# Kernel optimization log

Measured on AMD Instinct MI355X. Metric: run time of the kernel, lower is better.

## Reference

```python
import jax, jax.numpy as jnp
import numpy as np

N = 100_000      # target ('paper') nodes
E_RAND = 500_000 # random metapath edges (self-loops added on top)
C = 256          # channels
H = 8            # heads
D = C // H       # proj_dim = 32
SEM = 128        # semantic attention hidden
NEG_SLOPE = 0.2


def _edges(k):
    e = jax.random.randint(k, (2, E_RAND), 0, N, dtype=jnp.int32)
    loops = jnp.broadcast_to(jnp.arange(N, dtype=jnp.int32), (2, N))
    return jnp.concatenate([e, loops], axis=1)  # [2, E_RAND + N]


def setup_inputs() -> dict:
    key = jax.random.key(0)
    ks = jax.random.split(key, 9)
    return {
        "x": jax.random.normal(ks[0], (N, C), dtype=jnp.float32),
        "W": jax.random.normal(ks[1], (D, C), dtype=jnp.float32) * (1.0 / np.sqrt(C)),
        "att1": jax.random.normal(ks[2], (H, 2 * D), dtype=jnp.float32) * (1.0 / np.sqrt(2 * D)),
        "att2": jax.random.normal(ks[3], (H, 2 * D), dtype=jnp.float32) * (1.0 / np.sqrt(2 * D)),
        "fc_w": jax.random.normal(ks[4], (SEM, C), dtype=jnp.float32) * (1.0 / np.sqrt(C)),
        "fc_b": jnp.zeros((SEM,), dtype=jnp.float32),
        "q": jax.random.normal(ks[5], (SEM,), dtype=jnp.float32) * (1.0 / np.sqrt(SEM)),
        "ei1": _edges(ks[6]),
        "ei2": _edges(ks[7]),
    }


def _segment_softmax(e, dst, num_nodes):
    # numerically stable softmax over edges grouped by destination node
    m = jax.ops.segment_max(e, dst, num_segments=num_nodes)      # [N, H]
    ex = jnp.exp(e - m[dst])                                     # [E, H]
    s = jax.ops.segment_sum(ex, dst, num_segments=num_nodes)     # [N, H]
    return ex / s[dst]


def _gat_layer(h, ei, att):
    # h: [N, d] projected target features; ei: [2, E]; att: [H, 2d]
    src, dst = ei[0], ei[1]
    n, d = h.shape
    a_dst, a_src = att[:, :d], att[:, d:]   # cat order in torch: [h_i(dst), h_j(src)]
    # per-edge attention logits [E, H] without materializing [E, H, 2d]
    e = jax.nn.leaky_relu(h[dst] @ a_dst.T + h[src] @ a_src.T, NEG_SLOPE)
    alpha = _segment_softmax(e, dst, n)                          # [E, H]
    m = h[src][:, None, :] * alpha[:, :, None]                   # [E, H, d]
    out = jax.ops.segment_sum(m, dst, num_segments=n)            # [N, H, d]
    return jax.nn.elu(out).reshape(n, H * d)                     # [N, H*d]


def reference(x, W, att1, att2, fc_w, fc_b, q, ei1, ei2):
    # type-specific projection (bias-free Linear): [N, C] -> [N, d]
    h = x @ W.T
    Z1 = _gat_layer(h, ei1, att1)
    Z2 = _gat_layer(h, ei2, att2)
    # semantic attention across meta-paths
    def score(Z):
        return (jnp.tanh(Z @ fc_w.T + fc_b) @ q).mean()
    V = jax.nn.softmax(jnp.stack([score(Z1), score(Z2)]))        # [2]
    return V[0] * Z1 + V[1] * Z2                                 # [N, C]
```

## Files before the change

### kernel.cpp

```cpp
#include <hip/hip_runtime.h>
#include <math.h>

#define Nn 100000
#define Cc 256
#define Dd 32
#define Hh 8
#define SEMk 128
#define PAD 32
#define NEG 0.2f
#define NB1 25000
#define NTASK 12500

#if __has_builtin(__builtin_amdgcn_exp2f)
#define EXP2(x) __builtin_amdgcn_exp2f(x)
#else
#define EXP2(x) exp2f(x)
#endif
#define LOG2E 1.44269504088896f

typedef __attribute__((ext_vector_type(8))) short bf16x8;
typedef __attribute__((ext_vector_type(4))) short s16x4;
typedef __attribute__((ext_vector_type(4))) float f32x4;

__device__ __forceinline__ short f2bf(float f) {
    unsigned u = __float_as_uint(f);
    u = (u + 0x7FFF + ((u >> 16) & 1)) >> 16;
    return (short)u;
}

__global__ __launch_bounds__(256) void k_prep(const float* __restrict__ W,
                                              float* __restrict__ Wt,
                                              const float* __restrict__ fcw,
                                              short* __restrict__ fcwb) {
    int i = blockIdx.x * 256 + threadIdx.x;
    if (i < Dd * Cc) {
        int j = i >> 5, k = i & 31;
        Wt[i] = W[k * Cc + j];
    }
    if (i < SEMk * Cc) fcwb[i] = f2bf(fcw[i]);
}

__global__ __launch_bounds__(256) void k_hproj(const float* __restrict__ x,
                                               const float* __restrict__ Wt,
                                               const float* __restrict__ att1,
                                               const float* __restrict__ att2,
                                               float* __restrict__ h,
                                               float* __restrict__ sd1, float* __restrict__ ss1,
                                               float* __restrict__ sd2, float* __restrict__ ss2) {
    __shared__ float4 xs[32 * 65];
    __shared__ float  wt[256 * 36];
    __shared__ float4 hs[32 * 9];
    __shared__ float  a1[8 * 68];
    __shared__ float  a2[8 * 68];

    int t = threadIdx.x;
    int nb = blockIdx.x * 32;

    const float4* xg = (const float4*)x + (size_t)nb * 64;
#pragma unroll
    for (int it = 0; it < 8; ++it) {
        int i = t + it * 256;
        xs[(i >> 6) * 65 + (i & 63)] = xg[i];
    }
    const float4* wg = (const float4*)Wt;
#pragma unroll
    for (int it = 0; it < 8; ++it) {
        int i = t + it * 256;
        *(float4*)&wt[(i >> 3) * 36 + (i & 7) * 4] = wg[i];
    }
#pragma unroll
    for (int it = 0; it < 2; ++it) {
        int i = t + it * 256;
        a1[(i >> 6) * 68 + (i & 63)] = att1[i];
        a2[(i >> 6) * 68 + (i & 63)] = att2[i];
    }
    __syncthreads();

    int nl = t >> 3;
    int dq = t & 7;
    float4 acc = make_float4(0.f, 0.f, 0.f, 0.f);
    const float4* xr = &xs[nl * 65];
#pragma unroll 4
    for (int j4 = 0; j4 < 64; ++j4) {
        float4 xv = xr[j4];
        float4 w0 = *(const float4*)&wt[(j4 * 4 + 0) * 36 + dq * 4];
        float4 w1 = *(const float4*)&wt[(j4 * 4 + 1) * 36 + dq * 4];
        float4 w2 = *(const float4*)&wt[(j4 * 4 + 2) * 36 + dq * 4];
        float4 w3 = *(const float4*)&wt[(j4 * 4 + 3) * 36 + dq * 4];
        acc.x += xv.x * w0.x + xv.y * w1.x + xv.z * w2.x + xv.w * w3.x;
        acc.y += xv.x * w0.y + xv.y * w1.y + xv.z * w2.y + xv.w * w3.y;
        acc.z += xv.x * w0.z + xv.y * w1.z + xv.z * w2.z + xv.w * w3.z;
        acc.w += xv.x * w0.w + xv.y * w1.w + xv.z * w2.w + xv.w * w3.w;
    }
    ((float4*)h)[(size_t)(nb + nl) * 8 + dq] = acc;
    hs[nl * 9 + dq] = acc;
    __syncthreads();

    int nl2 = t >> 3;
    int hh = t & 7;
    float d1 = 0.f, s1 = 0.f, d2 = 0.f, s2 = 0.f;
#pragma unroll
    for (int d4 = 0; d4 < 8; ++d4) {
        float4 hv = hs[nl2 * 9 + d4];
        float4 ad1 = *(const float4*)&a1[hh * 68 + d4 * 4];
        float4 as1 = *(const float4*)&a1[hh * 68 + 32 + d4 * 4];
        float4 ad2 = *(const float4*)&a2[hh * 68 + d4 * 4];
        float4 as2 = *(const float4*)&a2[hh * 68 + 32 + d4 * 4];
        d1 += hv.x * ad1.x + hv.y * ad1.y + hv.z * ad1.z + hv.w * ad1.w;
        s1 += hv.x * as1.x + hv.y * as1.y + hv.z * as1.z + hv.w * as1.w;
        d2 += hv.x * ad2.x + hv.y * ad2.y + hv.z * ad2.z + hv.w * ad2.w;
        s2 += hv.x * as2.x + hv.y * as2.y + hv.z * as2.z + hv.w * as2.w;
    }
    int n = nb + nl2;
    sd1[n * 8 + hh] = d1 * LOG2E; ss1[n * 8 + hh] = s1 * LOG2E;
    sd2[n * 8 + hh] = d2 * LOG2E; ss2[n * 8 + hh] = s2 * LOG2E;
}

__global__ __launch_bounds__(256) void k_scatter(const int* __restrict__ ei1, int E1,
                                                 const int* __restrict__ ei2, int E2,
                                                 int* __restrict__ cnt,
                                                 int* __restrict__ slt1,
                                                 int* __restrict__ slt2) {
    int id = blockIdx.x * 256 + threadIdx.x;
    const int* ei; int e, EE; int* c; int* sl;
    if (id < E1) { ei = ei1; e = id; EE = E1; c = cnt; sl = slt1; }
    else {
        e = id - E1;
        if (e >= E2) return;
        ei = ei2; EE = E2; c = cnt + Nn; sl = slt2;
    }
    int s = ei[e];
    int d = ei[EE + e];
    int pos = atomicAdd(&c[d], 1);
    if (pos < PAD) sl[d * PAD + pos] = s;
}

#define LOADC(S0,S1,S2,S3,A0,A1,A2,A3,V0,V1,V2,V3,BB) do {                         \
    S0 = __shfl(sval, (BB) + 0); S1 = __shfl(sval, (BB) + 1);                      \
    S2 = __shfl(sval, (BB) + 2); S3 = __shfl(sval, (BB) + 3);                      \
    S1 = ((BB) + 1 < deg) ? S1 : n;                                                \
    S2 = ((BB) + 2 < deg) ? S2 : n;                                                \
    S3 = ((BB) + 3 < deg) ? S3 : n;                                                \
    A0 = ssrc[(unsigned)S0 * 8u + hh]; A1 = ssrc[(unsigned)S1 * 8u + hh];          \
    A2 = ssrc[(unsigned)S2 * 8u + hh]; A3 = ssrc[(unsigned)S3 * 8u + hh];          \
    V0 = h4[(unsigned)S0 * 8u + sub];  V1 = h4[(unsigned)S1 * 8u + sub];           \
    V2 = h4[(unsigned)S2 * 8u + sub];  V3 = h4[(unsigned)S3 * 8u + sub];           \
} while (0)

#define CONS(A0,A1,A2,A3,V0,V1,V2,V3,BB) do {                                      \
    float ev_, w_;                                                                 \
    ev_ = sd + A0; ev_ = ev_ > 0.f ? ev_ : NEG * ev_; w_ = EXP2(ev_);              \
    acc.x += w_ * V0.x; acc.y += w_ * V0.y; acc.z += w_ * V0.z; acc.w += w_ * V0.w; ssum += w_; \
    ev_ = sd + A1; ev_ = ev_ > 0.f ? ev_ : NEG * ev_; w_ = EXP2(ev_);              \
    w_ = ((BB) + 1 < deg) ? w_ : 0.f;                                              \
    acc.x += w_ * V1.x; acc.y += w_ * V1.y; acc.z += w_ * V1.z; acc.w += w_ * V1.w; ssum += w_; \
    ev_ = sd + A2; ev_ = ev_ > 0.f ? ev_ : NEG * ev_; w_ = EXP2(ev_);              \
    w_ = ((BB) + 2 < deg) ? w_ : 0.f;                                              \
    acc.x += w_ * V2.x; acc.y += w_ * V2.y; acc.z += w_ * V2.z; acc.w += w_ * V2.w; ssum += w_; \
    ev_ = sd + A3; ev_ = ev_ > 0.f ? ev_ : NEG * ev_; w_ = EXP2(ev_);              \
    w_ = ((BB) + 3 < deg) ? w_ : 0.f;                                              \
    acc.x += w_ * V3.x; acc.y += w_ * V3.y; acc.z += w_ * V3.z; acc.w += w_ * V3.w; ssum += w_; \
} while (0)

__global__ __launch_bounds__(256, 4) void k_gat(const float* __restrict__ h,
                                                const float* __restrict__ sd1, const float* __restrict__ ss1,
                                                const float* __restrict__ sd2, const float* __restrict__ ss2,
                                                const int* __restrict__ cnt,
                                                const int* __restrict__ slt1, const int* __restrict__ slt2,
                                                float* __restrict__ Z1, float* __restrict__ Z2) {
    int blk = blockIdx.x;
    const float* sdst = sd1; const float* ssrc = ss1;
    const int* cc = cnt; const int* sl = slt1; float* Z = Z1;
    if (blk >= NB1) { blk -= NB1; sdst = sd2; ssrc = ss2; cc = cnt + Nn; sl = slt2; Z = Z2; }
    int t = threadIdx.x;
    int lane = t & 63;
    int n = blk * 4 + (t >> 6);
    int deg = cc[n]; if (deg > PAD) deg = PAD;
    int hh = lane >> 3;
    int sub = lane & 7;
    float sd = sdst[n * 8 + hh];
    int sval = sl[n * PAD + (lane & 31)];
    const float4* h4 = (const float4*)h;

    float ssum = 0.f;
    float4 acc = make_float4(0.f, 0.f, 0.f, 0.f);

    int as0, as1, as2, as3;  float aa0, aa1, aa2, aa3;  float4 av0, av1, av2, av3;
    int bs0, bs1, bs2, bs3;  float ba0, ba1, ba2, ba3;  float4 bv0, bv1, bv2, bv3;

    LOADC(as0, as1, as2, as3, aa0, aa1, aa2, aa3, av0, av1, av2, av3, 0);
    int base = 0;
    for (;;) {
        int nxt = base + 4;
        bool more = nxt < deg;
        if (more) LOADC(bs0, bs1, bs2, bs3, ba0, ba1, ba2, ba3, bv0, bv1, bv2, bv3, nxt);
        CONS(aa0, aa1, aa2, aa3, av0, av1, av2, av3, base);
        if (!more) break;
        base = nxt;
        nxt = base + 4;
        more = nxt < deg;
        if (more) LOADC(as0, as1, as2, as3, aa0, aa1, aa2, aa3, av0, av1, av2, av3, nxt);
        CONS(ba0, ba1, ba2, ba3, bv0, bv1, bv2, bv3, base);
        if (!more) break;
        base = nxt;
    }

    float inv = 1.f / ssum;
    float4 o;
    o.x = acc.x * inv; o.y = acc.y * inv; o.z = acc.z * inv; o.w = acc.w * inv;
    o.x = o.x > 0.f ? o.x : __expf(o.x) - 1.f;
    o.y = o.y > 0.f ? o.y : __expf(o.y) - 1.f;
    o.z = o.z > 0.f ? o.z : __expf(o.z) - 1.f;
    o.w = o.w > 0.f ? o.w : __expf(o.w) - 1.f;
    ((float4*)Z)[(size_t)n * 64 + lane] = o;
}

__device__ __forceinline__ float fast_tanh(float x) {
    return 1.f - 2.f / (1.f + __expf(2.f * x));
}

#define SWZ(off, r) ((off) ^ (((r) & 7) << 4))

__global__ __launch_bounds__(256) void k_score(const float* __restrict__ Z1,
                        const float* __restrict__ Z2,
                        const short* __restrict__ fcwb,
                        const float* __restrict__ fcb,
                        const float* __restrict__ q,
                        float* __restrict__ Sacc) {
    __shared__ float zst[4 * 4096];
    int t = threadIdx.x;
    int lane = t & 63;
    int wid = t >> 6;
    int task = blockIdx.x * 4 + wid;
    const float* Z = Z1; float* bins = Sacc;
    int tile = task;
    if (task >= NTASK / 2) { Z = Z2; bins = Sacc + 256; tile = task - NTASK / 2; }
    int nodebase = tile * 16;
    float* myst = &zst[wid * 4096];

    const char* zb = (const char*)(Z + (size_t)nodebase * Cc);
#pragma unroll
    for (int r = 0; r < 16; ++r) {
        const char* src = zb + r * 1024 + SWZ(lane * 16, r);
        __builtin_amdgcn_global_load_lds(
            (const __attribute__((address_space(1))) void*)src,
            (__attribute__((address_space(3))) void*)(myst + r * 256),
            16, 0, 0);
    }
    asm volatile("s_waitcnt vmcnt(0)" ::: "memory");
    __builtin_amdgcn_sched_barrier(0);

    int col = lane & 15;
    int quad = lane >> 4;

    const char* rowp = (const char*)myst + col * 1024;
    bf16x8 af[8];
#pragma unroll
    for (int ks = 0; ks < 8; ++ks) {
        int b0 = ks * 128 + quad * 32;
        float4 f0 = *(const float4*)(rowp + SWZ(b0, col));
        float4 f1 = *(const float4*)(rowp + SWZ(b0 + 16, col));
        bf16x8 a;
        a[0] = f2bf(f0.x); a[1] = f2bf(f0.y); a[2] = f2bf(f0.z); a[3] = f2bf(f0.w);
        a[4] = f2bf(f1.x); a[5] = f2bf(f1.y); a[6] = f2bf(f1.z); a[7] = f2bf(f1.w);
        af[ks] = a;
    }

    f32x4 acc[8];
#pragma unroll
    for (int tt = 0; tt < 8; ++tt) { acc[tt][0] = 0.f; acc[tt][1] = 0.f; acc[tt][2] = 0.f; acc[tt][3] = 0.f; }

    const short* brow = fcwb + (size_t)col * Cc + quad * 8;
#pragma unroll
    for (int ks = 0; ks < 8; ++ks) {
        bf16x8 bf[8];
#pragma unroll
        for (int tt = 0; tt < 8; ++tt)
            bf[tt] = *(const bf16x8*)(brow + tt * 4096 + ks * 32);
#pragma unroll
        for (int tt = 0; tt < 8; ++tt)
            acc[tt] = __builtin_amdgcn_mfma_f32_16x16x32_bf16(af[ks], bf[tt], acc[tt], 0, 0, 0);
    }

    float local = 0.f;
#pragma unroll
    for (int tt = 0; tt < 8; ++tt) {
        int sem = tt * 16 + col;
        float b = fcb[sem], qq = q[sem];
#pragma unroll
        for (int r = 0; r < 4; ++r) local += fast_tanh(acc[tt][r] + b) * qq;
    }
#pragma unroll
    for (int off = 32; off > 0; off >>= 1) local += __shfl_down(local, off);
    if (lane == 0) atomicAdd(&bins[(task & 31) * 8], local);
}

__global__ __launch_bounds__(256) void k_combine(float* __restrict__ out,
                                                 const float* __restrict__ Z2,
                                                 const float* __restrict__ S) {
    float s1 = 0.f, s2 = 0.f;
#pragma unroll
    for (int i = 0; i < 32; ++i) { s1 += S[i * 8]; s2 += S[256 + i * 8]; }
    s1 *= (1.f / (float)Nn);
    s2 *= (1.f / (float)Nn);
    float mx = fmaxf(s1, s2);
    float e1 = __expf(s1 - mx), e2 = __expf(s2 - mx);
    float inv = 1.f / (e1 + e2);
    float V0 = e1 * inv, V1 = e2 * inv;
    size_t i = (size_t)blockIdx.x * 256 + threadIdx.x;
    if (i < (size_t)Nn * 64) {
        float4 a = ((float4*)out)[i];
        float4 b = ((const float4*)Z2)[i];
        a.x = V0 * a.x + V1 * b.x;
        a.y = V0 * a.y + V1 * b.y;
        a.z = V0 * a.z + V1 * b.z;
        a.w = V0 * a.w + V1 * b.w;
        ((float4*)out)[i] = a;
    }
}

extern "C" void kernel_launch(void* const* d_in, const int* in_sizes, int n_in,
                              void* d_out, int out_size, void* d_ws, size_t ws_size,
                              hipStream_t stream) {
    const float* x    = (const float*)d_in[0];
    const float* W    = (const float*)d_in[1];
    const float* att1 = (const float*)d_in[2];
    const float* att2 = (const float*)d_in[3];
    const float* fcw  = (const float*)d_in[4];
    const float* fcb  = (const float*)d_in[5];
    const float* q    = (const float*)d_in[6];
    const int*   ei1  = (const int*)d_in[7];
    const int*   ei2  = (const int*)d_in[8];
    int E1 = in_sizes[7] / 2;
    int E2 = in_sizes[8] / 2;
    float* out = (float*)d_out;

    char* ws = (char*)d_ws;
    size_t off = 0;
    auto alloc = [&](size_t bytes) -> char* {
        char* p = ws + off;
        off = (off + bytes + 255) & ~(size_t)255;
        return p;
    };
    float* Z2   = (float*)alloc((size_t)Nn * Cc * 4);
    float* h    = (float*)alloc((size_t)Nn * Dd * 4);
    float* sd1  = (float*)alloc((size_t)Nn * Hh * 4);
    float* ss1  = (float*)alloc((size_t)Nn * Hh * 4);
    float* sd2  = (float*)alloc((size_t)Nn * Hh * 4);
    float* ss2  = (float*)alloc((size_t)Nn * Hh * 4);
    int*   cnt  = (int*)alloc((size_t)2 * Nn * 4);
    float* red  = (float*)alloc(2048);
    float* Wt   = (float*)alloc((size_t)Dd * Cc * 4);
    short* fcwb = (short*)alloc((size_t)SEMk * Cc * 2);
    int*   slt1 = (int*)alloc((size_t)Nn * PAD * 4);
    int*   slt2 = (int*)alloc((size_t)Nn * PAD * 4);
    (void)ws_size; (void)n_in; (void)out_size;

    hipMemsetAsync(cnt, 0, (size_t)2 * Nn * 4, stream);
    hipMemsetAsync(red, 0, 2048, stream);

    k_prep<<<(SEMk * Cc + 255) / 256, 256, 0, stream>>>(W, Wt, fcw, fcwb);
    k_hproj<<<Nn / 32, 256, 0, stream>>>(x, Wt, att1, att2, h, sd1, ss1, sd2, ss2);
    k_scatter<<<(E1 + E2 + 255) / 256, 256, 0, stream>>>(ei1, E1, ei2, E2, cnt, slt1, slt2);
    k_gat<<<2 * NB1, 256, 0, stream>>>(h, sd1, ss1, sd2, ss2, cnt, slt1, slt2, out, Z2);
    k_score<<<NTASK / 4, 256, 0, stream>>>(out, Z2, fcwb, fcb, q, red);
    k_combine<<<(Nn * 64) / 256, 256, 0, stream>>>(out, Z2, red);
}
```

Before: 528.8 us.

## Fuse weight prep into scatter, register-block hproj over two nodes, use readlane

Merges the weight-transpose and bf16 conversion of fc_w into the edge scatter kernel, removing one kernel launch. k_hproj now runs 128 threads per block, and each thread computes two nodes so that every shared-memory weight load is reused twice. The LOADC macro now broadcasts source indices with readlane instead of shfl, which avoids LDS permute traffic, though it needs the lane index to be uniform across the wave. Fewer threads per block in hproj may lower latency hiding.

```diff
diff --git a/kernel.cpp b/kernel.cpp
--- a/kernel.cpp
+++ b/kernel.cpp
@@ -28,19 +28,37 @@
     return (short)u;
 }
 
-__global__ __launch_bounds__(256) void k_prep(const float* __restrict__ W,
-                                              float* __restrict__ Wt,
-                                              const float* __restrict__ fcw,
-                                              short* __restrict__ fcwb) {
-    int i = blockIdx.x * 256 + threadIdx.x;
-    if (i < Dd * Cc) {
-        int j = i >> 5, k = i & 31;
-        Wt[i] = W[k * Cc + j];
-    }
-    if (i < SEMk * Cc) fcwb[i] = f2bf(fcw[i]);
-}
-
-__global__ __launch_bounds__(256) void k_hproj(const float* __restrict__ x,
+__global__ __launch_bounds__(256) void k_scatter(const int* __restrict__ ei1, int E1,
+                                                 const int* __restrict__ ei2, int E2,
+                                                 int* __restrict__ cnt,
+                                                 int* __restrict__ slt1,
+                                                 int* __restrict__ slt2,
+                                                 const float* __restrict__ W,
+                                                 float* __restrict__ Wt,
+                                                 const float* __restrict__ fcw,
+                                                 short* __restrict__ fcwb) {
+    int id = blockIdx.x * 256 + threadIdx.x;
+    if (id < SEMk * Cc) {
+        if (id < Dd * Cc) {
+            int j = id >> 5, k = id & 31;
+            Wt[id] = W[k * Cc + j];
+        }
+        fcwb[id] = f2bf(fcw[id]);
+    }
+    const int* ei; int e, EE; int* c; int* sl;
+    if (id < E1) { ei = ei1; e = id; EE = E1; c = cnt; sl = slt1; }
+    else {
+        e = id - E1;
+        if (e >= E2) return;
+        ei = ei2; EE = E2; c = cnt + Nn; sl = slt2;
+    }
+    int s = ei[e];
+    int d = ei[EE + e];
+    int pos = atomicAdd(&c[d], 1);
+    if (pos < PAD) sl[d * PAD + pos] = s;
+}
+
+__global__ __launch_bounds__(128) void k_hproj(const float* __restrict__ x,
                                                const float* __restrict__ Wt,
                                                const float* __restrict__ att1,
                                                const float* __restrict__ att2,
@@ -58,86 +76,82 @@
 
     const float4* xg = (const float4*)x + (size_t)nb * 64;
 #pragma unroll
-    for (int it = 0; it < 8; ++it) {
-        int i = t + it * 256;
+    for (int it = 0; it < 16; ++it) {
+        int i = t + it * 128;
         xs[(i >> 6) * 65 + (i & 63)] = xg[i];
     }
     const float4* wg = (const float4*)Wt;
 #pragma unroll
-    for (int it = 0; it < 8; ++it) {
-        int i = t + it * 256;
+    for (int it = 0; it < 16; ++it) {
+        int i = t + it * 128;
         *(float4*)&wt[(i >> 3) * 36 + (i & 7) * 4] = wg[i];
     }
 #pragma unroll
-    for (int it = 0; it < 2; ++it) {
-        int i = t + it * 256;
+    for (int it = 0; it < 4; ++it) {
+        int i = t + it * 128;
         a1[(i >> 6) * 68 + (i & 63)] = att1[i];
         a2[(i >> 6) * 68 + (i & 63)] = att2[i];
     }
     __syncthreads();
 
-    int nl = t >> 3;
+    int np = t >> 3;
     int dq = t & 7;
-    float4 acc = make_float4(0.f, 0.f, 0.f, 0.f);
-    const float4* xr = &xs[nl * 65];
+    int n0 = np * 2, n1 = n0 + 1;
+    float4 acc0 = make_float4(0.f, 0.f, 0.f, 0.f);
+    float4 acc1 = make_float4(0.f, 0.f, 0.f, 0.f);
+    const float4* xr0 = &xs[n0 * 65];
+    const float4* xr1 = &xs[n1 * 65];
 #pragma unroll 4
     for (int j4 = 0; j4 < 64; ++j4) {
-        float4 xv = xr[j4];
+        float4 xv0 = xr0[j4];
+        float4 xv1 = xr1[j4];
         float4 w0 = *(const float4*)&wt[(j4 * 4 + 0) * 36 + dq * 4];
         float4 w1 = *(const float4*)&wt[(j4 * 4 + 1) * 36 + dq * 4];
         float4 w2 = *(const float4*)&wt[(j4 * 4 + 2) * 36 + dq * 4];
         float4 w3 = *(const float4*)&wt[(j4 * 4 + 3) * 36 + dq * 4];
-        acc.x += xv.x * w0.x + xv.y * w1.x + xv.z * w2.x + xv.w * w3.x;
-        acc.y += xv.x * w0.y + xv.y * w1.y + xv.z * w2.y + xv.w * w3.y;
-        acc.z += xv.x * w0.z + xv.y * w1.z + xv.z * w2.z + xv.w * w3.z;
-        acc.w += xv.x * w0.w + xv.y * w1.w + xv.z * w2.w + xv.w * w3.w;
-    }
-    ((float4*)h)[(size_t)(nb + nl) * 8 + dq] = acc;
-    hs[nl * 9 + dq] = acc;
+        acc0.x += xv0.x * w0.x + xv0.y * w1.x + xv0.z * w2.x + xv0.w * w3.x;
+        acc0.y += xv0.x * w0.y + xv0.y * w1.y + xv0.z * w2.y + xv0.w * w3.y;
+        acc0.z += xv0.x * w0.z + xv0.y * w1.z + xv0.z * w2.z + xv0.w * w3.z;
+        acc0.w += xv0.x * w0.w + xv0.y * w1.w + xv0.z * w2.w + xv0.w * w3.w;
+        acc1.x += xv1.x * w0.x + xv1.y * w1.x + xv1.z * w2.x + xv1.w * w3.x;
+        acc1.y += xv1.x * w0.y + xv1.y * w1.y + xv1.z * w2.y + xv1.w * w3.y;
+        acc1.z += xv1.x * w0.z + xv1.y * w1.z + xv1.z * w2.z + xv1.w * w3.z;
+        acc1.w += xv1.x * w0.w + xv1.y * w1.w + xv1.z * w2.w + xv1.w * w3.w;
+    }
+    ((float4*)h)[(size_t)(nb + n0) * 8 + dq] = acc0;
+    ((float4*)h)[(size_t)(nb + n1) * 8 + dq] = acc1;
+    hs[n0 * 9 + dq] = acc0;
+    hs[n1 * 9 + dq] = acc1;
     __syncthreads();
 
-    int nl2 = t >> 3;
     int hh = t & 7;
-    float d1 = 0.f, s1 = 0.f, d2 = 0.f, s2 = 0.f;
-#pragma unroll
-    for (int d4 = 0; d4 < 8; ++d4) {
-        float4 hv = hs[nl2 * 9 + d4];
-        float4 ad1 = *(const float4*)&a1[hh * 68 + d4 * 4];
-        float4 as1 = *(const float4*)&a1[hh * 68 + 32 + d4 * 4];
-        float4 ad2 = *(const float4*)&a2[hh * 68 + d4 * 4];
-        float4 as2 = *(const float4*)&a2[hh * 68 + 32 + d4 * 4];
-        d1 += hv.x * ad1.x + hv.y * ad1.y + hv.z * ad1.z + hv.w * ad1.w;
-        s1 += hv.x * as1.x + hv.y * as1.y + hv.z * as1.z + hv.w * as1.w;
-        d2 += hv.x * ad2.x + hv.y * ad2.y + hv.z * ad2.z + hv.w * ad2.w;
-        s2 += hv.x * as2.x + hv.y * as2.y + hv.z * as2.z + hv.w * as2.w;
-    }
-    int n = nb + nl2;
-    sd1[n * 8 + hh] = d1 * LOG2E; ss1[n * 8 + hh] = s1 * LOG2E;
-    sd2[n * 8 + hh] = d2 * LOG2E; ss2[n * 8 + hh] = s2 * LOG2E;
-}
-
-__global__ __launch_bounds__(256) void k_scatter(const int* __restrict__ ei1, int E1,
-                                                 const int* __restrict__ ei2, int E2,
-                                                 int* __restrict__ cnt,
-                                                 int* __restrict__ slt1,
-                                                 int* __restrict__ slt2) {
-    int id = blockIdx.x * 256 + threadIdx.x;
-    const int* ei; int e, EE; int* c; int* sl;
-    if (id < E1) { ei = ei1; e = id; EE = E1; c = cnt; sl = slt1; }
-    else {
-        e = id - E1;
-        if (e >= E2) return;
-        ei = ei2; EE = E2; c = cnt + Nn; sl = slt2;
-    }
-    int s = ei[e];
-    int d = ei[EE + e];
-    int pos = atomicAdd(&c[d], 1);
-    if (pos < PAD) sl[d * PAD + pos] = s;
+#pragma unroll
+    for (int rep = 0; rep < 2; ++rep) {
+        int nl2 = (t >> 3) * 2 + rep;
+        float d1 = 0.f, s1 = 0.f, d2 = 0.f, s2 = 0.f;
+#pragma unroll
+        for (int d4 = 0; d4 < 8; ++d4) {
+            float4 hv = hs[nl2 * 9 + d4];
+            float4 ad1 = *(const float4*)&a1[hh * 68 + d4 * 4];
+            float4 as1 = *(const float4*)&a1[hh * 68 + 32 + d4 * 4];
+            float4 ad2 = *(const float4*)&a2[hh * 68 + d4 * 4];
+            float4 as2 = *(const float4*)&a2[hh * 68 + 32 + d4 * 4];
+            d1 += hv.x * ad1.x + hv.y * ad1.y + hv.z * ad1.z + hv.w * ad1.w;
+            s1 += hv.x * as1.x + hv.y * as1.y + hv.z * as1.z + hv.w * as1.w;
+            d2 += hv.x * ad2.x + hv.y * ad2.y + hv.z * ad2.z + hv.w * ad2.w;
+            s2 += hv.x * as2.x + hv.y * as2.y + hv.z * as2.z + hv.w * as2.w;
+        }
+        int n = nb + nl2;
+        sd1[n * 8 + hh] = d1 * LOG2E; ss1[n * 8 + hh] = s1 * LOG2E;
+        sd2[n * 8 + hh] = d2 * LOG2E; ss2[n * 8 + hh] = s2 * LOG2E;
+    }
 }
 
 #define LOADC(S0,S1,S2,S3,A0,A1,A2,A3,V0,V1,V2,V3,BB) do {                         \
-    S0 = __shfl(sval, (BB) + 0); S1 = __shfl(sval, (BB) + 1);                      \
-    S2 = __shfl(sval, (BB) + 2); S3 = __shfl(sval, (BB) + 3);                      \
+    S0 = __builtin_amdgcn_readlane(sval, (BB) + 0);                                \
+    S1 = __builtin_amdgcn_readlane(sval, (BB) + 1);                                \
+    S2 = __builtin_amdgcn_readlane(sval, (BB) + 2);                                \
+    S3 = __builtin_amdgcn_readlane(sval, (BB) + 3);                                \
     S1 = ((BB) + 1 < deg) ? S1 : n;                                                \
     S2 = ((BB) + 2 < deg) ? S2 : n;                                                \
     S3 = ((BB) + 3 < deg) ? S3 : n;                                                \
@@ -359,9 +373,9 @@
     hipMemsetAsync(cnt, 0, (size_t)2 * Nn * 4, stream);
     hipMemsetAsync(red, 0, 2048, stream);
 
-    k_prep<<<(SEMk * Cc + 255) / 256, 256, 0, stream>>>(W, Wt, fcw, fcwb);
-    k_hproj<<<Nn / 32, 256, 0, stream>>>(x, Wt, att1, att2, h, sd1, ss1, sd2, ss2);
-    k_scatter<<<(E1 + E2 + 255) / 256, 256, 0, stream>>>(ei1, E1, ei2, E2, cnt, slt1, slt2);
+    k_scatter<<<(E1 + E2 + 255) / 256, 256, 0, stream>>>(ei1, E1, ei2, E2, cnt, slt1, slt2,
+                                                         W, Wt, fcw, fcwb);
+    k_hproj<<<Nn / 32, 128, 0, stream>>>(x, Wt, att1, att2, h, sd1, ss1, sd2, ss2);
     k_gat<<<2 * NB1, 256, 0, stream>>>(h, sd1, ss1, sd2, ss2, cnt, slt1, slt2, out, Z2);
     k_score<<<NTASK / 4, 256, 0, stream>>>(out, Z2, fcwb, fcb, q, red);
     k_combine<<<(Nn * 64) / 256, 256, 0, stream>>>(out, Z2, red);
```

After: 553.3 us. +4.6%, slower.
